# Performance work log

Hardware: AMD Instinct MI355X
Metric: run time of the kernel (lower is better)

## Reference

```python
import jax, jax.numpy as jnp
import numpy as np

N_NODES = 50000
N_EDGES = 640000
HID = 128
IN_DIM = 3
N_LAYERS = 4


def _silu(x):
    return x * jax.nn.sigmoid(x)


def setup_inputs() -> dict:
    key = jax.random.key(0)
    ks = jax.random.split(key, 20)
    s = 0.05
    inp = {
        'nodes': jax.random.normal(ks[0], (N_NODES, IN_DIM), jnp.float32),
        'edges': jax.random.randint(ks[1], (2, N_EDGES), 0, N_NODES, jnp.int32),
        'edge_attr': jax.random.normal(ks[2], (N_EDGES, 1), jnp.float32),
        # embedding: Linear(input_dim, hidden)
        'emb_w': jax.random.normal(ks[3], (IN_DIM, HID), jnp.float32) * s,
        'emb_b': jnp.zeros((HID,), jnp.float32),
        # per-layer GCL params (stacked over layers)
        # edge_mlp: Linear(2*HID + 1, HID) -> SiLU -> Linear(HID, HID) -> SiLU
        'edge_w1': jax.random.normal(ks[4], (N_LAYERS, 2 * HID + 1, HID), jnp.float32) * s,
        'edge_b1': jnp.zeros((N_LAYERS, HID), jnp.float32),
        'edge_w2': jax.random.normal(ks[5], (N_LAYERS, HID, HID), jnp.float32) * s,
        'edge_b2': jnp.zeros((N_LAYERS, HID), jnp.float32),
        # node_mlp: Linear(2*HID, HID) -> SiLU -> Linear(HID, HID)
        'node_w1': jax.random.normal(ks[6], (N_LAYERS, 2 * HID, HID), jnp.float32) * s,
        'node_b1': jnp.zeros((N_LAYERS, HID), jnp.float32),
        'node_w2': jax.random.normal(ks[7], (N_LAYERS, HID, HID), jnp.float32) * s,
        'node_b2': jnp.zeros((N_LAYERS, HID), jnp.float32),
        # decoder: Linear(HID, HID) -> SiLU -> Linear(HID, 3)
        'dec_w1': jax.random.normal(ks[8], (HID, HID), jnp.float32) * s,
        'dec_b1': jnp.zeros((HID,), jnp.float32),
        'dec_w2': jax.random.normal(ks[9], (HID, 3), jnp.float32) * s,
        'dec_b2': jnp.zeros((3,), jnp.float32),
    }
    return inp


def reference(nodes, edges, edge_attr, emb_w, emb_b,
              edge_w1, edge_b1, edge_w2, edge_b2,
              node_w1, node_b1, node_w2, node_b2,
              dec_w1, dec_b1, dec_w2, dec_b2):
    row, col = edges[0], edges[1]
    n = nodes.shape[0]
    h = nodes @ emb_w + emb_b  # [N, HID]
    for l in range(N_LAYERS):
        # edge model: gather endpoints, MLP on [h_src, h_tgt, edge_attr]
        e_in = jnp.concatenate([h[row], h[col], edge_attr], axis=1)  # [E, 2H+1]
        m = _silu(e_in @ edge_w1[l] + edge_b1[l])
        m = _silu(m @ edge_w2[l] + edge_b2[l])  # [E, HID]
        # node model: scatter-sum messages to source nodes, then MLP
        agg = jax.ops.segment_sum(m, row, num_segments=n)  # [N, HID]
        u = jnp.concatenate([h, agg], axis=1)
        u = _silu(u @ node_w1[l] + node_b1[l])
        h = u @ node_w2[l] + node_b2[l]  # recurrent=False: no residual
    out = _silu(h @ dec_w1 + dec_b1)
    return out @ dec_w2 + dec_b2  # [N, 3]
```

## Files before the change

kernel.cpp:

```cpp
#include <hip/hip_runtime.h>

#define N_NODES 50000
#define N_EDGES 640000
#define HID 128
#define N_LAYERS 4
#define TILE_E 128

typedef _Float16 f16x8 __attribute__((ext_vector_type(8)));
typedef float f32x16 __attribute__((ext_vector_type(16)));

__device__ __forceinline__ float silu_f(float x) {
    return x * __builtin_amdgcn_rcpf(1.0f + __expf(-x));
}

__device__ __forceinline__ f32x16 zero16() {
    f32x16 z;
#pragma unroll
    for (int i = 0; i < 16; ++i) z[i] = 0.f;
    return z;
}

__global__ void k_embed(const float* __restrict__ nodes, const float* __restrict__ ew,
                        const float* __restrict__ eb, float* __restrict__ h) {
    int idx = blockIdx.x * 256 + threadIdx.x;
    if (idx >= N_NODES * HID) return;
    int i = idx >> 7, c = idx & 127;
    float n0 = nodes[i * 3 + 0], n1 = nodes[i * 3 + 1], n2 = nodes[i * 3 + 2];
    h[idx] = n0 * ew[c] + n1 * ew[HID + c] + n2 * ew[2 * HID + c] + eb[c];
}

__global__ void k_hist(const int* __restrict__ row, int* __restrict__ deg) {
    int e = blockIdx.x * 256 + threadIdx.x;
    if (e < N_EDGES) atomicAdd(&deg[row[e]], 1);
}

__global__ __launch_bounds__(1024) void k_scan(const int* __restrict__ deg, int* __restrict__ off) {
    __shared__ int partial[1024];
    const int t = threadIdx.x;
    const int chunk = (N_NODES + 1023) / 1024;
    const int base = t * chunk;
    int s = 0;
    for (int i = 0; i < chunk; ++i) {
        int idx = base + i;
        if (idx < N_NODES) s += deg[idx];
    }
    partial[t] = s;
    __syncthreads();
    for (int o = 1; o < 1024; o <<= 1) {
        int v = (t >= o) ? partial[t - o] : 0;
        __syncthreads();
        partial[t] += v;
        __syncthreads();
    }
    int run = (t == 0) ? 0 : partial[t - 1];
    for (int i = 0; i < chunk; ++i) {
        int idx = base + i;
        if (idx < N_NODES) {
            off[idx] = run;
            run += deg[idx];
        }
    }
}

__global__ void k_scatter(const int* __restrict__ row, const int* __restrict__ col,
                          const float* __restrict__ ea, int* __restrict__ off,
                          int* __restrict__ row_s, int* __restrict__ col_s,
                          float* __restrict__ ea_s) {
    int e = blockIdx.x * 256 + threadIdx.x;
    if (e >= N_EDGES) return;
    int r = row[e];
    int pos = atomicAdd(&off[r], 1);
    row_s[pos] = r;
    col_s[pos] = col[e];
    ea_s[pos] = ea[e];
}

__global__ __launch_bounds__(256) void k_packW2(const float* __restrict__ W2all,
                                                _Float16* __restrict__ W2p) {
    const int layer = blockIdx.x;
    const float* W2 = W2all + (size_t)layer * 128 * 128;
    _Float16* out = W2p + (size_t)layer * 128 * 128;
    const int t = threadIdx.x;
    for (int fl = t; fl < 2048; fl += 256) {
        int blk = fl >> 6, lane = fl & 63;
        int cb = blk >> 3, kb = blk & 7;
        int colg = cb * 32 + (lane & 31);
        int kbase = kb * 16 + (lane >> 5) * 8;
        f16x8 v;
#pragma unroll
        for (int j = 0; j < 8; ++j)
            v[j] = (_Float16)W2[(size_t)(kbase + j) * 128 + colg];
        *(f16x8*)&out[(size_t)fl * 8] = v;
    }
}

__global__ __launch_bounds__(256) void k_packAll(
    const float* __restrict__ ew1, const float* __restrict__ nw1,
    const float* __restrict__ nw2, const float* __restrict__ dw1,
    _Float16* __restrict__ WpA, _Float16* __restrict__ WpB,
    _Float16* __restrict__ WpN1, _Float16* __restrict__ WpN2,
    _Float16* __restrict__ WpD1) {
    const int b = blockIdx.x;
    const float* W; _Float16* dst; int K16;
    if (b < 4)       { W = ew1 + (size_t)b * 257 * 128;              dst = WpA  + (size_t)b * 32768; K16 = 8; }
    else if (b < 8)  { int l = b - 4;  W = ew1 + (size_t)l * 257 * 128 + 128 * 128; dst = WpB + (size_t)l * 32768; K16 = 8; }
    else if (b < 12) { int l = b - 8;  W = nw1 + (size_t)l * 256 * 128; dst = WpN1 + (size_t)l * 65536; K16 = 16; }
    else if (b < 16) { int l = b - 12; W = nw2 + (size_t)l * 128 * 128; dst = WpN2 + (size_t)l * 32768; K16 = 8; }
    else             { W = dw1; dst = WpD1; K16 = 8; }
    for (int fl = threadIdx.x; fl < K16 * 256; fl += 256) {
        int lane = fl & 63, cb = (fl >> 6) & 3, ks = fl >> 8;
        int col = cb * 32 + (lane & 31);
        int kb = ks * 16 + (lane >> 5) * 8;
        f16x8 h8, l8;
#pragma unroll
        for (int j = 0; j < 8; ++j) {
            float wv = W[(size_t)(kb + j) * 128 + col];
            _Float16 hh = (_Float16)wv;
            h8[j] = hh;
            l8[j] = (_Float16)((wv - (float)hh) * 2048.0f);
        }
        *(f16x8*)&dst[((size_t)(0 * K16 + ks) * 4 + cb) * 512 + lane * 8] = h8;
        *(f16x8*)&dst[((size_t)(1 * K16 + ks) * 4 + cb) * 512 + lane * 8] = l8;
    }
}

__device__ __forceinline__ void split8(const float* xv, f16x8& xh, f16x8& xl) {
#pragma unroll
    for (int q = 0; q < 8; ++q) {
        _Float16 hh = (_Float16)xv[q];
        xh[q] = hh;
        xl[q] = (_Float16)((xv[q] - (float)hh) * 2048.0f);
    }
}

__global__ __launch_bounds__(512) void k_gemm3(
    const float* __restrict__ X1, const float* __restrict__ X2,
    const _Float16* __restrict__ Wp0, const float* __restrict__ bias0, float* __restrict__ out0,
    const _Float16* __restrict__ Wp1, const float* __restrict__ bias1, float* __restrict__ out1,
    int M, int K16, int do_silu) {
    const int t = threadIdx.x, w = t >> 6, l = t & 63;
    const int lane31 = l & 31, hi = l >> 5;
    const bool dual = (Wp1 != nullptr);
    int rb, cb0, sel;
    if (dual) { rb = w & 1; sel = w >> 2; cb0 = ((w >> 1) & 1) * 2; }
    else      { rb = w & 3; sel = 0;      cb0 = (w >> 2) * 2; }
    const int mtile = dual ? 64 : 128;
    const int m0 = blockIdx.x * mtile;
    const _Float16* Wp = sel ? Wp1 : Wp0;
    const float* bias = sel ? bias1 : bias0;
    float* out = sel ? out1 : out0;

    int rowg = m0 + rb * 32 + lane31;
    if (rowg >= M) rowg = M - 1;
    const int koff = hi * 8;

    f32x16 aH0 = zero16(), aH1 = zero16(), aL0 = zero16(), aL1 = zero16();
    const f16x8* Wv = (const f16x8*)Wp;
#pragma unroll 4
    for (int ks = 0; ks < K16; ++ks) {
        const float* Xp = (X2 != nullptr && ks >= 8) ? X2 : X1;
        const float* px = &Xp[(size_t)rowg * 128 + (ks & 7) * 16 + koff];
        float xv[8];
        *(float4*)&xv[0] = *(const float4*)px;
        *(float4*)&xv[4] = *(const float4*)(px + 4);
        f16x8 xh, xl;
        split8(xv, xh, xl);
        f16x8 bh0 = Wv[((size_t)ks * 4 + cb0) * 64 + l];
        f16x8 bh1 = Wv[((size_t)ks * 4 + cb0 + 1) * 64 + l];
        f16x8 bl0 = Wv[((size_t)(K16 + ks) * 4 + cb0) * 64 + l];
        f16x8 bl1 = Wv[((size_t)(K16 + ks) * 4 + cb0 + 1) * 64 + l];
        aH0 = __builtin_amdgcn_mfma_f32_32x32x16_f16(xh, bh0, aH0, 0, 0, 0);
        aH1 = __builtin_amdgcn_mfma_f32_32x32x16_f16(xh, bh1, aH1, 0, 0, 0);
        aL0 = __builtin_amdgcn_mfma_f32_32x32x16_f16(xh, bl0, aL0, 0, 0, 0);
        aL0 = __builtin_amdgcn_mfma_f32_32x32x16_f16(xl, bh0, aL0, 0, 0, 0);
        aL1 = __builtin_amdgcn_mfma_f32_32x32x16_f16(xh, bl1, aL1, 0, 0, 0);
        aL1 = __builtin_amdgcn_mfma_f32_32x32x16_f16(xl, bh1, aL1, 0, 0, 0);
    }
    const float inv = 1.0f / 2048.0f;
#pragma unroll
    for (int c = 0; c < 2; ++c) {
        int col = (cb0 + c) * 32 + lane31;
        float bv = bias ? bias[col] : 0.f;
        const f32x16& aH = c ? aH1 : aH0;
        const f32x16& aL = c ? aL1 : aL0;
#pragma unroll
        for (int r = 0; r < 16; ++r) {
            int gr = m0 + rb * 32 + (r & 3) + 8 * (r >> 2) + 4 * hi;
            if (gr < M) {
                float v = aH[r] + aL[r] * inv + bv;
                out[(size_t)gr * 128 + col] = do_silu ? silu_f(v) : v;
            }
        }
    }
}

__global__ __launch_bounds__(512) void k_node(
    float* __restrict__ h, const float* __restrict__ agg,
    const _Float16* __restrict__ Wn1, const float* __restrict__ nb1,
    const _Float16* __restrict__ Wn2, const float* __restrict__ nb2,
    const _Float16* __restrict__ WA, const float* __restrict__ ebA,
    const _Float16* __restrict__ WB,
    float* __restrict__ outA, float* __restrict__ outB,
    const _Float16* __restrict__ WD, const float* __restrict__ db1,
    const float* __restrict__ dw2, const float* __restrict__ db2,
    float* __restrict__ dec_out, int M, int final_mode) {
    __shared__ float u_lds[128 * 133];
    __shared__ float w2l[384];
    const int t = threadIdx.x, w = t >> 6, l = t & 63;
    const int lane31 = l & 31, hi = l >> 5;
    const int rb = w & 3, cb0 = (w >> 2) * 2;
    const int m0 = blockIdx.x * 128;
    const int koff = hi * 8;
    const float inv = 1.0f / 2048.0f;

    if (final_mode && t < 384) w2l[t] = dw2[t];

    int rowg = m0 + rb * 32 + lane31;
    if (rowg >= M) rowg = M - 1;

    {
        f32x16 aH0 = zero16(), aH1 = zero16(), aL0 = zero16(), aL1 = zero16();
        const f16x8* Wv = (const f16x8*)Wn1;
#pragma unroll 4
        for (int ks = 0; ks < 16; ++ks) {
            const float* Xp = (ks >= 8) ? agg : h;
            const float* px = &Xp[(size_t)rowg * 128 + (ks & 7) * 16 + koff];
            float xv[8];
            *(float4*)&xv[0] = *(const float4*)px;
            *(float4*)&xv[4] = *(const float4*)(px + 4);
            f16x8 xh, xl;
            split8(xv, xh, xl);
            f16x8 bh0 = Wv[((size_t)ks * 4 + cb0) * 64 + l];
            f16x8 bh1 = Wv[((size_t)ks * 4 + cb0 + 1) * 64 + l];
            f16x8 bl0 = Wv[((size_t)(16 + ks) * 4 + cb0) * 64 + l];
            f16x8 bl1 = Wv[((size_t)(16 + ks) * 4 + cb0 + 1) * 64 + l];
            aH0 = __builtin_amdgcn_mfma_f32_32x32x16_f16(xh, bh0, aH0, 0, 0, 0);
            aH1 = __builtin_amdgcn_mfma_f32_32x32x16_f16(xh, bh1, aH1, 0, 0, 0);
            aL0 = __builtin_amdgcn_mfma_f32_32x32x16_f16(xh, bl0, aL0, 0, 0, 0);
            aL0 = __builtin_amdgcn_mfma_f32_32x32x16_f16(xl, bh0, aL0, 0, 0, 0);
            aL1 = __builtin_amdgcn_mfma_f32_32x32x16_f16(xh, bl1, aL1, 0, 0, 0);
            aL1 = __builtin_amdgcn_mfma_f32_32x32x16_f16(xl, bh1, aL1, 0, 0, 0);
        }
#pragma unroll
        for (int c = 0; c < 2; ++c) {
            int col = (cb0 + c) * 32 + lane31;
            float bv = nb1[col];
            const f32x16& aH = c ? aH1 : aH0;
            const f32x16& aL = c ? aL1 : aL0;
#pragma unroll
            for (int r = 0; r < 16; ++r) {
                int lr = rb * 32 + (r & 3) + 8 * (r >> 2) + 4 * hi;
                u_lds[lr * 133 + col] = silu_f(aH[r] + aL[r] * inv + bv);
            }
        }
    }
    __syncthreads();

    {
        f32x16 aH0 = zero16(), aH1 = zero16(), aL0 = zero16(), aL1 = zero16();
        const f16x8* Wv = (const f16x8*)Wn2;
#pragma unroll
        for (int ks = 0; ks < 8; ++ks) {
            float xv[8];
            const int base = (rb * 32 + lane31) * 133 + ks * 16 + koff;
#pragma unroll
            for (int q = 0; q < 8; ++q) xv[q] = u_lds[base + q];
            f16x8 xh, xl;
            split8(xv, xh, xl);
            f16x8 bh0 = Wv[((size_t)ks * 4 + cb0) * 64 + l];
            f16x8 bh1 = Wv[((size_t)ks * 4 + cb0 + 1) * 64 + l];
            f16x8 bl0 = Wv[((size_t)(8 + ks) * 4 + cb0) * 64 + l];
            f16x8 bl1 = Wv[((size_t)(8 + ks) * 4 + cb0 + 1) * 64 + l];
            aH0 = __builtin_amdgcn_mfma_f32_32x32x16_f16(xh, bh0, aH0, 0, 0, 0);
            aH1 = __builtin_amdgcn_mfma_f32_32x32x16_f16(xh, bh1, aH1, 0, 0, 0);
            aL0 = __builtin_amdgcn_mfma_f32_32x32x16_f16(xh, bl0, aL0, 0, 0, 0);
            aL0 = __builtin_amdgcn_mfma_f32_32x32x16_f16(xl, bh0, aL0, 0, 0, 0);
            aL1 = __builtin_amdgcn_mfma_f32_32x32x16_f16(xh, bl1, aL1, 0, 0, 0);
            aL1 = __builtin_amdgcn_mfma_f32_32x32x16_f16(xl, bh1, aL1, 0, 0, 0);
        }
        __syncthreads();
#pragma unroll
        for (int c = 0; c < 2; ++c) {
            int col = (cb0 + c) * 32 + lane31;
            float bv = nb2[col];
            const f32x16& aH = c ? aH1 : aH0;
            const f32x16& aL = c ? aL1 : aL0;
#pragma unroll
            for (int r = 0; r < 16; ++r) {
                int lr = rb * 32 + (r & 3) + 8 * (r >> 2) + 4 * hi;
                float v = aH[r] + aL[r] * inv + bv;
                u_lds[lr * 133 + col] = v;
                int gr = m0 + lr;
                if (!final_mode && gr < M) h[(size_t)gr * 128 + col] = v;
            }
        }
    }
    __syncthreads();

    if (!final_mode) {
#pragma unroll
        for (int pass = 0; pass < 2; ++pass) {
            const int sel = w >> 2, w2 = w & 3;
            const int cbp = w2 >> 1, cb0p = (cbp) * 2;
            const int rb3 = (w2 & 1) * 2 + pass;
            const _Float16* Wp = sel ? WB : WA;
            float* op = sel ? outB : outA;
            f32x16 aH0 = zero16(), aH1 = zero16(), aL0 = zero16(), aL1 = zero16();
            const f16x8* Wv = (const f16x8*)Wp;
#pragma unroll
            for (int ks = 0; ks < 8; ++ks) {
                float xv[8];
                const int base = (rb3 * 32 + lane31) * 133 + ks * 16 + koff;
#pragma unroll
                for (int q = 0; q < 8; ++q) xv[q] = u_lds[base + q];
                f16x8 xh, xl;
                split8(xv, xh, xl);
                f16x8 bh0 = Wv[((size_t)ks * 4 + cb0p) * 64 + l];
                f16x8 bh1 = Wv[((size_t)ks * 4 + cb0p + 1) * 64 + l];
                f16x8 bl0 = Wv[((size_t)(8 + ks) * 4 + cb0p) * 64 + l];
                f16x8 bl1 = Wv[((size_t)(8 + ks) * 4 + cb0p + 1) * 64 + l];
                aH0 = __builtin_amdgcn_mfma_f32_32x32x16_f16(xh, bh0, aH0, 0, 0, 0);
                aH1 = __builtin_amdgcn_mfma_f32_32x32x16_f16(xh, bh1, aH1, 0, 0, 0);
                aL0 = __builtin_amdgcn_mfma_f32_32x32x16_f16(xh, bl0, aL0, 0, 0, 0);
                aL0 = __builtin_amdgcn_mfma_f32_32x32x16_f16(xl, bh0, aL0, 0, 0, 0);
                aL1 = __builtin_amdgcn_mfma_f32_32x32x16_f16(xh, bl1, aL1, 0, 0, 0);
                aL1 = __builtin_amdgcn_mfma_f32_32x32x16_f16(xl, bh1, aL1, 0, 0, 0);
            }
#pragma unroll
            for (int c = 0; c < 2; ++c) {
                int col = (cb0p + c) * 32 + lane31;
                float bv = sel ? 0.f : ebA[col];
                const f32x16& aH = c ? aH1 : aH0;
                const f32x16& aL = c ? aL1 : aL0;
#pragma unroll
                for (int r = 0; r < 16; ++r) {
                    int gr = m0 + rb3 * 32 + (r & 3) + 8 * (r >> 2) + 4 * hi;
                    if (gr < M) op[(size_t)gr * 128 + col] = aH[r] + aL[r] * inv + bv;
                }
            }
        }
    } else {
        f32x16 aH0 = zero16(), aH1 = zero16(), aL0 = zero16(), aL1 = zero16();
        const f16x8* Wv = (const f16x8*)WD;
#pragma unroll
        for (int ks = 0; ks < 8; ++ks) {
            float xv[8];
            const int base = (rb * 32 + lane31) * 133 + ks * 16 + koff;
#pragma unroll
            for (int q = 0; q < 8; ++q) xv[q] = u_lds[base + q];
            f16x8 xh, xl;
            split8(xv, xh, xl);
            f16x8 bh0 = Wv[((size_t)ks * 4 + cb0) * 64 + l];
            f16x8 bh1 = Wv[((size_t)ks * 4 + cb0 + 1) * 64 + l];
            f16x8 bl0 = Wv[((size_t)(8 + ks) * 4 + cb0) * 64 + l];
            f16x8 bl1 = Wv[((size_t)(8 + ks) * 4 + cb0 + 1) * 64 + l];
            aH0 = __builtin_amdgcn_mfma_f32_32x32x16_f16(xh, bh0, aH0, 0, 0, 0);
            aH1 = __builtin_amdgcn_mfma_f32_32x32x16_f16(xh, bh1, aH1, 0, 0, 0);
            aL0 = __builtin_amdgcn_mfma_f32_32x32x16_f16(xh, bl0, aL0, 0, 0, 0);
            aL0 = __builtin_amdgcn_mfma_f32_32x32x16_f16(xl, bh0, aL0, 0, 0, 0);
            aL1 = __builtin_amdgcn_mfma_f32_32x32x16_f16(xh, bl1, aL1, 0, 0, 0);
            aL1 = __builtin_amdgcn_mfma_f32_32x32x16_f16(xl, bh1, aL1, 0, 0, 0);
        }
        __syncthreads();
#pragma unroll
        for (int c = 0; c < 2; ++c) {
            int col = (cb0 + c) * 32 + lane31;
            float bv = db1[col];
            const f32x16& aH = c ? aH1 : aH0;
            const f32x16& aL = c ? aL1 : aL0;
#pragma unroll
            for (int r = 0; r < 16; ++r) {
                int lr = rb * 32 + (r & 3) + 8 * (r >> 2) + 4 * hi;
                u_lds[lr * 133 + col] = silu_f(aH[r] + aL[r] * inv + bv);
            }
        }
        __syncthreads();
        if (t < 384) {
            int rowl = t & 127, j = t >> 7;
            int gm = m0 + rowl;
            if (gm < M) {
                float s = db2[j];
                for (int c = 0; c < 128; ++c)
                    s += u_lds[rowl * 133 + c] * w2l[c * 3 + j];
                dec_out[(size_t)gm * 3 + j] = s;
            }
        }
    }
}

__global__ __launch_bounds__(512, 4) void k_edge4(
    const float* __restrict__ A, const float* __restrict__ Bm,
    const float* __restrict__ w1last, const float* __restrict__ b2,
    const _Float16* __restrict__ W2p, const int* __restrict__ row_s,
    const int* __restrict__ col_s, const float* __restrict__ ea_s,
    float* __restrict__ agg) {
    __shared__ __align__(16) _Float16 W2s[16384];
    __shared__ __align__(16) _Float16 m1f[TILE_E * 136];
    __shared__ int rows_sh[TILE_E];
    __shared__ int segs_sh[TILE_E + 2];
    __shared__ unsigned long long masks_sh[2];

    const int t = threadIdx.x;
    const int w = t >> 6, l = t & 63;
    const int lane31 = l & 31, hi = l >> 5;

    for (int i = t; i < 2048; i += 512)
        ((float4*)W2s)[i] = ((const float4*)W2p)[i];

    const int e_mine = (w >> 1) * 32 + lane31;
    const int kbase0 = (w & 1) * 64 + hi * 8;

    const int rb_g = w & 3;
    const int cb0 = (w >> 2) * 2, cb1 = cb0 + 1;
    const float b20 = b2[cb0 * 32 + lane31];
    const float b21 = b2[cb1 * 32 + lane31];

    const f16x8* m1v = (const f16x8*)m1f;
    const f16x8* w2v = (const f16x8*)W2s;
    _Float16* mo = m1f;

    const int n_tiles = N_EDGES / TILE_E;
    const int stride = gridDim.x;

    int r_pf = 0; float ea_pf = 0.f;
    float bpf[32];

    auto issue_pf = [&](int tile) {
        int eg = tile * TILE_E + e_mine;
        r_pf = row_s[eg];
        int c = col_s[eg];
        ea_pf = ea_s[eg];
        const float* Bp = Bm + (size_t)c * 128;
#pragma unroll
        for (int j = 0; j < 4; ++j) {
            int k0 = kbase0 + j * 16;
            *(float4*)&bpf[j * 8] = *(const float4*)&Bp[k0];
            *(float4*)&bpf[j * 8 + 4] = *(const float4*)&Bp[k0 + 4];
        }
    };

    int tile = blockIdx.x;
    if (tile < n_tiles) issue_pf(tile);

    for (; tile < n_tiles; tile += stride) {
        __syncthreads();

        {
            const int r = r_pf;
            const float eav = ea_pf;
            const float* Ap = A + (size_t)r * 128;
#pragma unroll
            for (int j = 0; j < 4; ++j) {
                int k0 = kbase0 + j * 16;
                float av[8], wv_[8];
                *(float4*)&av[0] = *(const float4*)&Ap[k0];
                *(float4*)&av[4] = *(const float4*)&Ap[k0 + 4];
                *(float4*)&wv_[0] = *(const float4*)&w1last[k0];
                *(float4*)&wv_[4] = *(const float4*)&w1last[k0 + 4];
                f16x8 o;
#pragma unroll
                for (int q = 0; q < 8; ++q)
                    o[q] = (_Float16)silu_f(av[q] + bpf[j * 8 + q] + eav * wv_[q]);
                *(f16x8*)&m1f[(w * 4 + j) * 512 + l * 8] = o;
            }
            if ((w & 1) == 0 && hi == 0) rows_sh[e_mine] = r;
        }
        __syncthreads();

        if (t < 128) {
            bool flag = (t == 0) || (rows_sh[t] != rows_sh[t - 1]);
            unsigned long long m = __ballot(flag);
            if ((t & 63) == 0) masks_sh[t >> 6] = m;
        }

        int nt = tile + stride;
        if (nt < n_tiles) issue_pf(nt);

        f32x16 acc0 = zero16(), acc1 = zero16();
#pragma unroll
        for (int kb = 0; kb < 8; ++kb) {
            f16x8 a = m1v[(rb_g * 8 + kb) * 64 + l];
            acc0 = __builtin_amdgcn_mfma_f32_32x32x16_f16(a, w2v[(cb0 * 8 + kb) * 64 + l], acc0, 0, 0, 0);
            acc1 = __builtin_amdgcn_mfma_f32_32x32x16_f16(a, w2v[(cb1 * 8 + kb) * 64 + l], acc1, 0, 0, 0);
        }
        __syncthreads();

        const unsigned long long m0 = masks_sh[0], m1m = masks_sh[1];
        const int ns = __popcll(m0) + __popcll(m1m);
        if (t < 128) {
            bool bit = (t < 64) ? ((m0 >> t) & 1ull) : ((m1m >> (t - 64)) & 1ull);
            if (bit) {
                int idx = (t < 64) ? __popcll(m0 & ((1ull << t) - 1))
                                   : __popcll(m0) + __popcll(m1m & ((1ull << (t - 64)) - 1));
                segs_sh[idx] = t;
            }
        }
        if (t == 0) segs_sh[ns] = TILE_E;

#pragma unroll
        for (int r = 0; r < 16; ++r) {
            int rowi = (r & 3) + 8 * (r >> 2) + 4 * hi;
            int erow = rb_g * 32 + rowi;
            mo[erow * 136 + cb0 * 32 + lane31] = (_Float16)silu_f(acc0[r] + b20);
            mo[erow * 136 + cb1 * 32 + lane31] = (_Float16)silu_f(acc1[r] + b21);
        }
        __syncthreads();

        {
            const int c = t & 127, g = t >> 7;
            for (int s = g; s < ns; s += 4) {
                int st = segs_sh[s], en = segs_sh[s + 1];
                float sum = 0.f;
                for (int q = st; q < en; ++q) sum += (float)mo[q * 136 + c];
                atomicAdd(&agg[(size_t)rows_sh[st] * 128 + c], sum);
            }
        }
    }
}

extern "C" void kernel_launch(void* const* d_in, const int* in_sizes, int n_in,
                              void* d_out, int out_size, void* d_ws, size_t ws_size,
                              hipStream_t stream) {
    const float* nodes = (const float*)d_in[0];
    const int* edges = (const int*)d_in[1];
    const float* ea = (const float*)d_in[2];
    const float* emb_w = (const float*)d_in[3];
    const float* emb_b = (const float*)d_in[4];
    const float* ew1 = (const float*)d_in[5];
    const float* eb1 = (const float*)d_in[6];
    const float* ew2 = (const float*)d_in[7];
    const float* eb2 = (const float*)d_in[8];
    const float* nw1 = (const float*)d_in[9];
    const float* nb1 = (const float*)d_in[10];
    const float* nw2 = (const float*)d_in[11];
    const float* nb2 = (const float*)d_in[12];
    const float* dw1 = (const float*)d_in[13];
    const float* db1 = (const float*)d_in[14];
    const float* dw2 = (const float*)d_in[15];
    const float* db2 = (const float*)d_in[16];
    const int* row = edges;
    const int* col = edges + N_EDGES;

    const size_t NH = (size_t)N_NODES * HID;
    float* r0 = (float*)d_ws;
    float* r1 = r0 + NH;
    float* r2 = r1 + NH;
    float* r3 = r2 + NH;
    int* deg = (int*)(r3 + NH);
    int* off = deg + N_NODES;
    int* row_s = off + N_NODES;
    int* col_s = row_s + N_EDGES;
    float* ea_s = (float*)(col_s + N_EDGES);
    _Float16* W2p = (_Float16*)(ea_s + N_EDGES);
    _Float16* WpA  = W2p  + (size_t)4 * 16384;
    _Float16* WpB  = WpA  + (size_t)4 * 32768;
    _Float16* WpN1 = WpB  + (size_t)4 * 32768;
    _Float16* WpN2 = WpN1 + (size_t)4 * 65536;
    _Float16* WpD1 = WpN2 + (size_t)4 * 32768;

    hipMemsetAsync(deg, 0, N_NODES * sizeof(int), stream);
    k_hist<<<(N_EDGES + 255) / 256, 256, 0, stream>>>(row, deg);
    k_scan<<<1, 1024, 0, stream>>>(deg, off);
    k_scatter<<<(N_EDGES + 255) / 256, 256, 0, stream>>>(row, col, ea, off, row_s, col_s, ea_s);
    k_packW2<<<N_LAYERS, 256, 0, stream>>>(ew2, W2p);
    k_packAll<<<17, 256, 0, stream>>>(ew1, nw1, nw2, dw1, WpA, WpB, WpN1, WpN2, WpD1);

    k_embed<<<(N_NODES * HID + 255) / 256, 256, 0, stream>>>(nodes, emb_w, emb_b, r0);

    const int g64 = (N_NODES + 63) / 64;
    const int g128 = (N_NODES + 127) / 128;

    k_gemm3<<<g64, 512, 0, stream>>>(r0, nullptr,
                                     WpA, eb1, r1,
                                     WpB, nullptr, r2,
                                     N_NODES, 8, 0);

    for (int l = 0; l < N_LAYERS; ++l) {
        hipMemsetAsync(r3, 0, NH * sizeof(float), stream);
        k_edge4<<<512, 512, 0, stream>>>(r1, r2,
                                         ew1 + (size_t)l * 257 * 128 + 256 * 128,
                                         eb2 + l * 128,
                                         W2p + (size_t)l * 16384,
                                         row_s, col_s, ea_s, r3);
        if (l < N_LAYERS - 1) {
            k_node<<<g128, 512, 0, stream>>>(r0, r3,
                                             WpN1 + (size_t)l * 65536, nb1 + l * 128,
                                             WpN2 + (size_t)l * 32768, nb2 + l * 128,
                                             WpA + (size_t)(l + 1) * 32768, eb1 + (l + 1) * 128,
                                             WpB + (size_t)(l + 1) * 32768,
                                             r1, r2,
                                             nullptr, nullptr, nullptr, nullptr, nullptr,
                                             N_NODES, 0);
        } else {
            k_node<<<g128, 512, 0, stream>>>(r0, r3,
                                             WpN1 + (size_t)l * 65536, nb1 + l * 128,
                                             WpN2 + (size_t)l * 32768, nb2 + l * 128,
                                             nullptr, nullptr, nullptr,
                                             nullptr, nullptr,
                                             WpD1, db1, dw2, db2,
                                             (float*)d_out, N_NODES, 1);
        }
    }
}
```

Measured before the change: 952.5 us.

## Reduce edge messages in registers with per-wave segment sums instead of LDS staging

The edge kernel now keeps the second-layer SiLU outputs in MFMA accumulators and performs the segmented sum over sorted source rows within each wave, using ballot, shuffle and ffs to find segment boundaries before issuing atomics. This removes the LDS write-back of messages, the shared-memory segment-table construction and two block barriers per tile. It also reassigns warps so each wave computes its own 32 edges across a K half. In exchange, segments spanning 32-edge wave blocks produce more atomics, and every segment loops over all 16 accumulator rows with masking. The launch bounds' min-blocks hint is also dropped.

```diff
diff --git a/kernel.cpp b/kernel.cpp
--- a/kernel.cpp
+++ b/kernel.cpp
@@ -388,17 +388,27 @@
     }
 }
 
-__global__ __launch_bounds__(512, 4) void k_edge4(
+#define EPI9(ACC, BV) { _Pragma("unroll") \
+    for (int rr = 0; rr < 16; ++rr) ACC[rr] = silu_f(ACC[rr] + BV); }
+
+#define SEGSUM9(ACC, CB) { \
+    float p = 0.f; \
+    _Pragma("unroll") \
+    for (int rr = 0; rr < 16; ++rr) { \
+        int erow = (rr & 3) + 8 * (rr >> 2) + 4 * hi; \
+        p += (erow >= st && erow < en) ? ACC[rr] : 0.f; \
+    } \
+    p += __shfl_xor(p, 32); \
+    if (hi == 0) atomicAdd(&agg[(size_t)rseg * 128 + (CB) * 32 + lane31], p); }
+
+__global__ __launch_bounds__(512) void k_edge9(
     const float* __restrict__ A, const float* __restrict__ Bm,
     const float* __restrict__ w1last, const float* __restrict__ b2,
     const _Float16* __restrict__ W2p, const int* __restrict__ row_s,
     const int* __restrict__ col_s, const float* __restrict__ ea_s,
     float* __restrict__ agg) {
     __shared__ __align__(16) _Float16 W2s[16384];
-    __shared__ __align__(16) _Float16 m1f[TILE_E * 136];
-    __shared__ int rows_sh[TILE_E];
-    __shared__ int segs_sh[TILE_E + 2];
-    __shared__ unsigned long long masks_sh[2];
+    __shared__ __align__(16) _Float16 m1f[16384];
 
     const int t = threadIdx.x;
     const int w = t >> 6, l = t & 63;
@@ -407,17 +417,16 @@
     for (int i = t; i < 2048; i += 512)
         ((float4*)W2s)[i] = ((const float4*)W2p)[i];
 
-    const int e_mine = (w >> 1) * 32 + lane31;
-    const int kbase0 = (w & 1) * 64 + hi * 8;
-
-    const int rb_g = w & 3;
-    const int cb0 = (w >> 2) * 2, cb1 = cb0 + 1;
+    const int rb = w & 3;
+    const int kh = w >> 2;
+    const int kbase0 = kh * 64 + hi * 8;
+    const int cb0 = kh * 2, cb1 = cb0 + 1;
     const float b20 = b2[cb0 * 32 + lane31];
     const float b21 = b2[cb1 * 32 + lane31];
+    const int e_mine = rb * 32 + lane31;
 
     const f16x8* m1v = (const f16x8*)m1f;
     const f16x8* w2v = (const f16x8*)W2s;
-    _Float16* mo = m1f;
 
     const int n_tiles = N_EDGES / TILE_E;
     const int stride = gridDim.x;
@@ -446,9 +455,8 @@
         __syncthreads();
 
         {
-            const int r = r_pf;
             const float eav = ea_pf;
-            const float* Ap = A + (size_t)r * 128;
+            const float* Ap = A + (size_t)r_pf * 128;
 #pragma unroll
             for (int j = 0; j < 4; ++j) {
                 int k0 = kbase0 + j * 16;
@@ -461,58 +469,37 @@
 #pragma unroll
                 for (int q = 0; q < 8; ++q)
                     o[q] = (_Float16)silu_f(av[q] + bpf[j * 8 + q] + eav * wv_[q]);
-                *(f16x8*)&m1f[(w * 4 + j) * 512 + l * 8] = o;
-            }
-            if ((w & 1) == 0 && hi == 0) rows_sh[e_mine] = r;
-        }
-        __syncthreads();
-
-        if (t < 128) {
-            bool flag = (t == 0) || (rows_sh[t] != rows_sh[t - 1]);
-            unsigned long long m = __ballot(flag);
-            if ((t & 63) == 0) masks_sh[t >> 6] = m;
-        }
-
+                *(f16x8*)&m1f[(rb * 8 + (k0 >> 4)) * 512 + l * 8] = o;
+            }
+        }
+        __syncthreads();
+
+        const int r_cur = r_pf;
         int nt = tile + stride;
         if (nt < n_tiles) issue_pf(nt);
 
         f32x16 acc0 = zero16(), acc1 = zero16();
 #pragma unroll
         for (int kb = 0; kb < 8; ++kb) {
-            f16x8 a = m1v[(rb_g * 8 + kb) * 64 + l];
+            f16x8 a = m1v[(rb * 8 + kb) * 64 + l];
             acc0 = __builtin_amdgcn_mfma_f32_32x32x16_f16(a, w2v[(cb0 * 8 + kb) * 64 + l], acc0, 0, 0, 0);
             acc1 = __builtin_amdgcn_mfma_f32_32x32x16_f16(a, w2v[(cb1 * 8 + kb) * 64 + l], acc1, 0, 0, 0);
         }
-        __syncthreads();
-
-        const unsigned long long m0 = masks_sh[0], m1m = masks_sh[1];
-        const int ns = __popcll(m0) + __popcll(m1m);
-        if (t < 128) {
-            bool bit = (t < 64) ? ((m0 >> t) & 1ull) : ((m1m >> (t - 64)) & 1ull);
-            if (bit) {
-                int idx = (t < 64) ? __popcll(m0 & ((1ull << t) - 1))
-                                   : __popcll(m0) + __popcll(m1m & ((1ull << (t - 64)) - 1));
-                segs_sh[idx] = t;
-            }
-        }
-        if (t == 0) segs_sh[ns] = TILE_E;
-
-#pragma unroll
-        for (int r = 0; r < 16; ++r) {
-            int rowi = (r & 3) + 8 * (r >> 2) + 4 * hi;
-            int erow = rb_g * 32 + rowi;
-            mo[erow * 136 + cb0 * 32 + lane31] = (_Float16)silu_f(acc0[r] + b20);
-            mo[erow * 136 + cb1 * 32 + lane31] = (_Float16)silu_f(acc1[r] + b21);
-        }
-        __syncthreads();
-
+
+        EPI9(acc0, b20) EPI9(acc1, b21)
         {
-            const int c = t & 127, g = t >> 7;
-            for (int s = g; s < ns; s += 4) {
-                int st = segs_sh[s], en = segs_sh[s + 1];
-                float sum = 0.f;
-                for (int q = st; q < en; ++q) sum += (float)mo[q * 136 + c];
-                atomicAdd(&agg[(size_t)rows_sh[st] * 128 + c], sum);
+            int prev = __shfl_up(r_cur, 1, 32);
+            bool flag = (lane31 == 0) || (r_cur != prev);
+            unsigned mask = (unsigned)__ballot(flag);
+            int ns = __popc(mask);
+            unsigned mrem = mask;
+            for (int s = 0; s < ns; ++s) {
+                int st = __ffs(mrem) - 1;
+                unsigned mnext = mrem & (mrem - 1);
+                int en = mnext ? (__ffs(mnext) - 1) : 32;
+                mrem = mnext;
+                int rseg = __shfl(r_cur, st, 32);
+                SEGSUM9(acc0, cb0) SEGSUM9(acc1, cb1)
             }
         }
     }
@@ -577,7 +564,7 @@
 
     for (int l = 0; l < N_LAYERS; ++l) {
         hipMemsetAsync(r3, 0, NH * sizeof(float), stream);
-        k_edge4<<<512, 512, 0, stream>>>(r1, r2,
+        k_edge9<<<512, 512, 0, stream>>>(r1, r2,
                                          ew1 + (size_t)l * 257 * 128 + 256 * 128,
                                          eb2 + l * 128,
                                          W2p + (size_t)l * 16384,
```

After: 1.014 ms. +6.4%, slower.
